# Optimization experiments

Hardware: AMD Instinct MI355X
Metric: run time of the kernel (lower is better)

Reference implementation:

```python
import jax, jax.numpy as jnp
import numpy as np

T_FRAMES = 8          # hardcoded in forward: T = int(8)
MAX_DISP = 3          # Correlation(kernel_size=1, max_displacement=3)
NUM_HEADS = 8
EPS = 1e-12           # F.normalize default eps


def setup_inputs() -> dict:
    key = jax.random.key(0)
    k1, k2, k3 = jax.random.split(key, 3)
    B, N, C = 2, 8192, 512  # N = T*H*W = 8*32*32
    x = jax.random.normal(k1, (B, N, C), jnp.float32)
    w_qkv = jax.random.normal(k2, (3 * C, C), jnp.float32) * (C ** -0.5)
    w_proj = jax.random.normal(k3, (C, C), jnp.float32) * (C ** -0.5)
    b_proj = jnp.zeros((C,), jnp.float32)
    return {"x": x, "w_qkv": w_qkv, "w_proj": w_proj, "b_proj": b_proj}


def _correlation(q, k, max_disp):
    # FlowNet-style cost volume, kernel_size=1: for each displacement (dy,dx)
    # in [-max_disp, max_disp]^2, mean over channels of q[.,h,w]*k[.,h+dy,w+dx],
    # out-of-bounds reads of k are zero. q,k: (b, d, H, W) -> (b, (2m+1)^2, H, W)
    b, d, H, W = q.shape
    kpad = jnp.pad(k, ((0, 0), (0, 0), (max_disp, max_disp), (max_disp, max_disp)))
    outs = []
    for dy in range(2 * max_disp + 1):
        for dx in range(2 * max_disp + 1):
            ks = kpad[:, :, dy:dy + H, dx:dx + W]
            outs.append(jnp.sum(q * ks, axis=1))
    return jnp.stack(outs, axis=1) / d


def _l2norm_ch(x):
    # normalize over channel axis 1 (F.normalize(dim=1))
    n = jnp.sqrt(jnp.sum(x * x, axis=1, keepdims=True))
    return x / jnp.maximum(n, EPS)


def reference(x, w_qkv, w_proj, b_proj):
    B, N, C = x.shape
    heads = NUM_HEADS
    hd = C // heads
    T = T_FRAMES
    H = int(round((N // T) ** 0.5)); W = H
    U = (2 * MAX_DISP + 1) ** 2  # 49

    qkv = (x @ w_qkv.T).reshape(B, N, 3, heads, hd).transpose(2, 0, 3, 1, 4)
    q, k, v = qkv[0], qkv[1], qkv[2]  # (B, heads, N, hd)

    # (b n) t d h w layout
    q = q.reshape(B * heads, T, H, W, hd).transpose(0, 1, 4, 2, 3)
    k = k.reshape(B * heads, T, H, W, hd).transpose(0, 1, 4, 2, 3)
    v = v.reshape(B * heads * T, H * W, hd)

    # k_postfix: shift k one frame earlier in time, repeat last frame
    k_post = jnp.concatenate([k[:, 1:], k[:, -1:]], axis=1)

    qf = _l2norm_ch(q.reshape(B * heads * T, hd, H, W))
    kf = _l2norm_ch(k_post.reshape(B * heads * T, hd, H, W))

    corr = _correlation(qf, kf, MAX_DISP).reshape(B * heads * T, U, H * W)
    # motion_attn = corr^T @ corr over the displacement axis, softmax over keys
    attn = jax.nn.softmax(jnp.einsum('bui,buj->bij', corr, corr), axis=-1)
    out = jnp.einsum('bij,bjd->bid', attn, v)  # (B*heads*T, H*W, hd)

    out = out.reshape(B, heads, T * H * W, hd).transpose(0, 2, 1, 3).reshape(B, N, C)
    return out @ w_proj.T + b_proj
```

## Files before the change

### kernel.cpp

```cpp
#include <hip/hip_runtime.h>
#include <hip/hip_bf16.h>
#include <stdint.h>


#define DEVFN __device__ __forceinline__

typedef __attribute__((ext_vector_type(8))) short bf16x8;
typedef __attribute__((ext_vector_type(4))) short s16x4;
typedef __attribute__((ext_vector_type(4))) float f32x4;

DEVFN float bf2f(short s) {
  union { unsigned int u; float f; } v;
  v.u = ((unsigned int)(unsigned short)s) << 16;
  return v.f;
}
DEVFN short f2bf(float f) {
  __hip_bfloat16 h = __float2bfloat16(f);
  return *reinterpret_cast<short*>(&h);
}

DEVFN void gl_lds16(const void* g, void* l) {
  __builtin_amdgcn_global_load_lds((const __attribute__((address_space(1))) void*)g,
                                   (__attribute__((address_space(3))) void*)l, 16, 0, 0);
}

#define MFMA(a, b, c) __builtin_amdgcn_mfma_f32_16x16x32_bf16((a), (b), (c), 0, 0, 0)

#define NTOK 8192
#define HW   1024

__global__ void k_cvt3(const float* __restrict__ x, const float* __restrict__ wq,
                       const float* __restrict__ wp, short* __restrict__ xb,
                       short* __restrict__ wqb, short* __restrict__ wpb) {
  int pid = blockIdx.x;
  const float* in; short* out; int i;
  if (pid < 4096)      { in = x;  out = xb;  i = pid * 256 + threadIdx.x; }
  else if (pid < 4480) { in = wq; out = wqb; i = (pid - 4096) * 256 + threadIdx.x; }
  else                 { in = wp; out = wpb; i = (pid - 4480) * 256 + threadIdx.x; }
  const float4* p = (const float4*)in + (size_t)i * 2;
  float4 a = p[0], b = p[1];
  bf16x8 r;
  r[0]=f2bf(a.x); r[1]=f2bf(a.y); r[2]=f2bf(a.z); r[3]=f2bf(a.w);
  r[4]=f2bf(b.x); r[5]=f2bf(b.y); r[6]=f2bf(b.z); r[7]=f2bf(b.w);
  *(bf16x8*)(out + (size_t)i * 8) = r;
}

template<int F32OUT>
__global__ __launch_bounds__(256, 2) void k_gemm_bt(
    const short* __restrict__ A, const short* __restrict__ Bm,
    void* __restrict__ Cp, const float* __restrict__ bias, int M, int N, int K)
{
  __shared__ short lA[128 * 64];
  __shared__ short lB[128 * 64];
  const int tid = threadIdx.x;
  const int lane = tid & 63, w = tid >> 6;
  const int wm = w >> 1, wn = w & 1;
  const int r15 = lane & 15, hi = (lane >> 4) * 16, g4 = (lane >> 4) * 4;
  const int pid = blockIdx.x;
  const int m0 = ((pid & 7) * 16 + ((pid >> 3) & 15)) * 128;
  const int n0 = (pid >> 7) * 128;

  f32x4 acc[4][4];
#pragma unroll
  for (int i = 0; i < 4; i++)
#pragma unroll
    for (int j = 0; j < 4; j++) acc[i][j] = (f32x4)0.f;

  for (int k0 = 0; k0 < K; k0 += 64) {
#pragma unroll
    for (int it = 0; it < 4; it++) {
      int chunk = it * 256 + tid;
      int row = chunk >> 3;
      int sb = ((chunk & 7) * 16) ^ ((row & 7) << 4);
      const char* srcA = (const char*)(A + (size_t)(m0 + row) * K + k0) + sb;
      const char* srcB = (const char*)(Bm + (size_t)(n0 + row) * K + k0) + sb;
      gl_lds16(srcA, lA + (it * 256 + w * 64) * 8);
      gl_lds16(srcB, lB + (it * 256 + w * 64) * 8);
    }
    asm volatile("s_waitcnt vmcnt(0)" ::: "memory");
    __syncthreads();

    bf16x8 af[4][2], bfr[4][2];
#pragma unroll
    for (int mt = 0; mt < 4; mt++) {
      int row = wm * 64 + mt * 16 + r15;
#pragma unroll
      for (int kh = 0; kh < 2; kh++) {
        int off = row * 128 + ((kh * 64 + hi) ^ ((row & 7) << 4));
        af[mt][kh] = *(const bf16x8*)((const char*)lA + off);
      }
    }
#pragma unroll
    for (int nt = 0; nt < 4; nt++) {
      int row = wn * 64 + nt * 16 + r15;
#pragma unroll
      for (int kh = 0; kh < 2; kh++) {
        int off = row * 128 + ((kh * 64 + hi) ^ ((row & 7) << 4));
        bfr[nt][kh] = *(const bf16x8*)((const char*)lB + off);
      }
    }
#pragma unroll
    for (int mt = 0; mt < 4; mt++)
#pragma unroll
      for (int nt = 0; nt < 4; nt++) {
        acc[mt][nt] = MFMA(af[mt][0], bfr[nt][0], acc[mt][nt]);
        acc[mt][nt] = MFMA(af[mt][1], bfr[nt][1], acc[mt][nt]);
      }
    __syncthreads();
  }

#pragma unroll
  for (int mt = 0; mt < 4; mt++)
#pragma unroll
    for (int j = 0; j < 4; j++) {
      int row = m0 + wm * 64 + mt * 16 + g4 + j;
#pragma unroll
      for (int nt = 0; nt < 4; nt++) {
        int col = n0 + wn * 64 + nt * 16 + r15;
        float v = acc[mt][nt][j];
        if (F32OUT) ((float*)Cp)[(size_t)row * N + col] = v + bias[col];
        else        ((short*)Cp)[(size_t)row * N + col] = f2bf(v);
      }
    }
}

__global__ __launch_bounds__(256, 4) void k_norm(short* __restrict__ qkvb) {
  const int tid = threadIdx.x;
  const int pid = blockIdx.x;
  const int xcd = pid & 7, idx = pid >> 3;
  const int g = 2 * xcd + (idx & 1);
  const int slice = (idx >> 1) & 1;
  const int iblk = idx >> 2;
#pragma unroll 1
  for (int pass = 0; pass < 8; ++pass) {
    int unit = pass * 32 + (tid >> 3);
    int i = iblk * 32 + (unit >> 3);
    int h = unit & 7;
    size_t addr = ((size_t)(g * HW + i)) * 1536 + slice * 512 + h * 64 + (tid & 7) * 8;
    bf16x8 d = *(const bf16x8*)(qkvb + addr);
    float ss = 0.f;
#pragma unroll
    for (int e = 0; e < 8; e++) { float f = bf2f(d[e]); ss += f * f; }
    ss += __shfl_xor(ss, 1); ss += __shfl_xor(ss, 2); ss += __shfl_xor(ss, 4);
    float sc = 1.f / (8.f * fmaxf(sqrtf(ss), 1e-12f));
    bf16x8 o;
#pragma unroll
    for (int e = 0; e < 8; e++) o[e] = f2bf(bf2f(d[e]) * sc);
    *(bf16x8*)(qkvb + addr) = o;
  }
}

__global__ __launch_bounds__(512, 4) void k_corr(
    const short* __restrict__ qkvb, short* __restrict__ corrI, short* __restrict__ corrU)
{
  __shared__ short stg[2560 * 8];
  __shared__ short scr[28 * 256];

  const int tid = threadIdx.x;
  const int lane = tid & 63, w = tid >> 6;
  const int r15 = lane & 15, hi = (lane >> 4) * 16, g4 = (lane >> 4) * 4;
  const int pid = blockIdx.x;
  const int xcd = pid & 7, idx = pid >> 3;
  const int g = 2 * xcd + (idx & 1);
  const int head = (idx >> 1) & 7;
  const int y0 = (idx >> 4) * 2;
  const int b = g >> 3, tf = g & 7;
  const int bht = b * 64 + head * 8 + tf;
  const int tk = (tf < 7) ? tf + 1 : 7;
  const size_t qbase = ((size_t)(g * HW)) * 1536 + head * 64;
  const size_t kbase = ((size_t)((b * 8 + tk) * HW)) * 1536 + 512 + head * 64;

#pragma unroll
  for (int i = 0; i < 5; i++) {
    int c = i * 512 + tid;
    int row = c >> 3;
    int sb = ((c & 7) * 16) ^ ((row & 7) << 4);
    short* dst = stg + (i * 512 + w * 64) * 8;
    if (i == 0) {
      int j = c >> 8, px = (c >> 3) & 31;
      gl_lds16((const char*)(qkvb + qbase + (size_t)((y0 + j) * 32 + px) * 1536) + sb, dst);
    } else {
      int c2 = c - 512;
      int slot = c2 >> 8, px = (c2 >> 3) & 31;
      int r = y0 - 3 + slot;
      if (r >= 0 && r < 32)
        gl_lds16((const char*)(qkvb + kbase + (size_t)(r * 32 + px) * 1536) + sb, dst);
      else
        *(bf16x8*)(stg + (size_t)c * 8) = (bf16x8)(short)0;
    }
  }
  asm volatile("s_waitcnt vmcnt(0)" ::: "memory");
  __syncthreads();

#pragma unroll 1
  for (int j = 0; j < 2; j++) {
    const int y = y0 + j;
    if (w < 7) {
      bf16x8 aq[2][2];
#pragma unroll
      for (int mt = 0; mt < 2; mt++) {
        int row = j * 32 + mt * 16 + r15;
#pragma unroll
        for (int kh = 0; kh < 2; kh++) {
          int off = row * 128 + ((kh * 64 + hi) ^ ((row & 7) << 4));
          aq[mt][kh] = *(const bf16x8*)((const char*)stg + off);
        }
      }
#pragma unroll
      for (int c = 0; c < 4; c++) {
        int t = w * 4 + c, nt = t >> 1, mt = t & 1;
        int dy = nt >> 1, xh = nt & 1;
        int slot = dy + j;
        int xx = xh * 16 + r15;
        int rowB = 64 + slot * 32 + xx;
        f32x4 a = (f32x4)0.f;
#pragma unroll
        for (int kh = 0; kh < 2; kh++) {
          int off = rowB * 128 + ((kh * 64 + hi) ^ ((rowB & 7) << 4));
          bf16x8 bb = *(const bf16x8*)((const char*)stg + off);
          a = MFMA(aq[mt][kh], bb, a);
        }
        s16x4 pk;
        pk[0] = f2bf(a[0]); pk[1] = f2bf(a[1]); pk[2] = f2bf(a[2]); pk[3] = f2bf(a[3]);
        *(s16x4*)(scr + t * 256 + r15 * 16 + g4) = pk;
      }
    }
    __syncthreads();

    if (tid < 256) {
      int x = tid >> 3, u0 = (tid & 7) * 8;
      bf16x8 o;
#pragma unroll
      for (int e = 0; e < 8; e++) {
        int u = u0 + e;
        int dy = u >> 3, dx = u & 7;
        int xx = x + dx - 3;
        int dyc = (dy > 6) ? 6 : dy;
        int t2 = (dyc * 2 + ((xx & 31) >> 4)) * 2 + (x >> 4);
        short vv = scr[t2 * 256 + (xx & 15) * 16 + (x & 15)];
        bool ok = (dx < 7) && (dy < 7) && (xx >= 0) && (xx < 32);
        short res = ok ? vv : (short)0;
        o[e] = (u == 63) ? (short)0x3F80 : res;
      }
      *(bf16x8*)(corrI + ((size_t)bht * HW + y * 32 + x) * 64 + u0) = o;
    } else {
      int tt = tid - 256;
      int u = tt >> 2, x0 = (tt & 3) * 8;
      int dy = u >> 3, dx = u & 7;
      int dyc = (dy > 6) ? 6 : dy;
      bf16x8 o;
#pragma unroll
      for (int e = 0; e < 8; e++) {
        int x = x0 + e;
        int xx = x + dx - 3;
        int t2 = (dyc * 2 + ((xx & 31) >> 4)) * 2 + (x >> 4);
        short vv = scr[t2 * 256 + (xx & 15) * 16 + (x & 15)];
        bool ok = (dx < 7) && (dy < 7) && (xx >= 0) && (xx < 32);
        short res = ok ? vv : (short)0;
        o[e] = (u == 63) ? (short)0x3F80 : res;
      }
      *(bf16x8*)(corrU + (size_t)bht * 65536 + u * HW + y * 32 + x0) = o;
    }
    __syncthreads();
  }
}

__global__ __launch_bounds__(256, 2) void k_vT(const short* __restrict__ qkvb, short* __restrict__ vT)
{
  __shared__ short lt[128 * 72];
  const int tid = threadIdx.x;
  const int pid = blockIdx.x;
  const int xcd = pid & 7, idx = pid >> 3;
  const int g = 2 * xcd + (idx & 1);
  const int head = (idx >> 1) & 7;
  const int cbase = (idx >> 4) * 256;
  const int b = g >> 3, tf = g & 7;
  const int bht = b * 64 + head * 8 + tf;
  const size_t rowbase = ((size_t)(g * HW)) * 1536 + 1024 + head * 64;
  for (int c0 = cbase; c0 < cbase + 256; c0 += 128) {
    __syncthreads();
#pragma unroll
    for (int it = 0; it < 4; it++) {
      int idx2 = it * 256 + tid;
      int row = idx2 >> 3, part = idx2 & 7;
      bf16x8 v = *(const bf16x8*)(qkvb + rowbase + (size_t)(c0 + row) * 1536 + part * 8);
      *(bf16x8*)(lt + row * 72 + part * 8) = v;
    }
    __syncthreads();
    int d = tid & 63, blk = tid >> 6;
#pragma unroll
    for (int qq = 0; qq < 4; qq++) {
      bf16x8 o;
#pragma unroll
      for (int e = 0; e < 8; e++) o[e] = lt[(blk * 32 + qq * 8 + e) * 72 + d];
      *(bf16x8*)(vT + ((size_t)bht * 64 + d) * HW + c0 + blk * 32 + qq * 8) = o;
    }
  }
}

__global__ __launch_bounds__(256, 2) void k_attn(
    const short* __restrict__ corrU, const short* __restrict__ corrI,
    const short* __restrict__ vT, short* __restrict__ out_attn)
{
  __shared__ short lV[32 * 64];
  __shared__ short lU[64 * 64];
  __shared__ short GTl[32 * 72];
  __shared__ float cl[64];
  __shared__ float cpart[256];
  const int tid = threadIdx.x, lane = tid & 63, w = tid >> 6;
  const int r15 = lane & 15, hi = (lane >> 4) * 16, g4 = (lane >> 4) * 4, g8 = (lane >> 4) * 8;
  const int pid = blockIdx.x;
  const int xcd = pid & 7, idx = pid >> 3;
  const int g = 2 * xcd + (idx & 1);
  const int head = (idx >> 1) & 7;
  const int dh = (idx >> 4) & 1;
  const int b = g >> 3, tf = g & 7;
  const int bht = b * 64 + head * 8 + tf;
  const int wm = w & 1, wn2 = (w >> 1) * 2;

  f32x4 accP[2];
  accP[0] = (f32x4)0.f; accP[1] = (f32x4)0.f;
  float c1p = 0.f;
  const short* vbase = vT + ((size_t)bht * 64 + dh * 32) * HW;
  const short* ubase = corrU + (size_t)bht * 65536;

  for (int i0 = 0; i0 < 1024; i0 += 64) {
    { int row = tid >> 3;
      int sb = ((tid & 7) * 16) ^ ((row & 7) << 4);
      gl_lds16((const char*)(vbase + (size_t)row * HW + i0) + sb, lV + (w * 64) * 8);
    }
#pragma unroll
    for (int it = 0; it < 2; it++) {
      int chunk = it * 256 + tid;
      int row = chunk >> 3;
      int sb = ((chunk & 7) * 16) ^ ((row & 7) << 4);
      gl_lds16((const char*)(ubase + (size_t)row * HW + i0) + sb, lU + (it * 256 + w * 64) * 8);
    }
    asm volatile("s_waitcnt vmcnt(0)" ::: "memory");
    __syncthreads();
    bf16x8 av[2];
    int rowA = wm * 16 + r15;
#pragma unroll
    for (int kh = 0; kh < 2; kh++) {
      int off = rowA * 128 + ((kh * 64 + hi) ^ ((rowA & 7) << 4));
      av[kh] = *(const bf16x8*)((const char*)lV + off);
    }
#pragma unroll
    for (int c = 0; c < 2; c++) {
      int rowB = (wn2 + c) * 16 + r15;
#pragma unroll
      for (int kh = 0; kh < 2; kh++) {
        int off = rowB * 128 + ((kh * 64 + hi) ^ ((rowB & 7) << 4));
        bf16x8 bu = *(const bf16x8*)((const char*)lU + off);
        accP[c] = MFMA(av[kh], bu, accP[c]);
      }
    }
    { int u = tid >> 2, partc = tid & 3;
#pragma unroll
      for (int h = 0; h < 2; h++) {
        int off = u * 128 + ((partc * 32 + h * 16) ^ ((u & 7) << 4));
        bf16x8 vv = *(const bf16x8*)((const char*)lU + off);
#pragma unroll
        for (int e = 0; e < 8; e++) c1p += bf2f(vv[e]);
      }
    }
    __syncthreads();
  }
  cpart[tid] = c1p;
#pragma unroll
  for (int c = 0; c < 2; c++)
#pragma unroll
    for (int j = 0; j < 4; j++) {
      int d = wm * 16 + g4 + j, u = (wn2 + c) * 16 + r15;
      GTl[d * 72 + u] = f2bf(accP[c][j]);
    }
  __syncthreads();
  if (tid < 64) cl[tid] = cpart[4 * tid] + cpart[4 * tid + 1] + cpart[4 * tid + 2] + cpart[4 * tid + 3];
  __syncthreads();

  bf16x8 gtb[2][2];
#pragma unroll
  for (int nt = 0; nt < 2; nt++)
#pragma unroll
    for (int kh = 0; kh < 2; kh++)
      gtb[nt][kh] = *(const bf16x8*)((const char*)GTl + (nt * 16 + r15) * 144 + kh * 64 + hi);

  float c1r[2][8];
#pragma unroll
  for (int kh = 0; kh < 2; kh++)
#pragma unroll
    for (int e = 0; e < 8; e++) c1r[kh][e] = cl[kh * 32 + g8 + e];

  const short* ibase = corrI + (size_t)bht * HW * 64;
  for (int s = 0; s < 16; s++) {
    int i0 = w * 256 + s * 16;
    bf16x8 af[2];
#pragma unroll
    for (int kh = 0; kh < 2; kh++)
      af[kh] = *(const bf16x8*)(ibase + (size_t)(i0 + r15) * 64 + kh * 32 + g8);
    f32x4 a2[2];
    a2[0] = (f32x4)0.f; a2[1] = (f32x4)0.f;
#pragma unroll
    for (int nt = 0; nt < 2; nt++)
#pragma unroll
      for (int kh = 0; kh < 2; kh++) a2[nt] = MFMA(af[kh], gtb[nt][kh], a2[nt]);

    float dp = 0.f;
#pragma unroll
    for (int kh = 0; kh < 2; kh++)
#pragma unroll
      for (int e = 0; e < 8; e++) dp += bf2f(af[kh][e]) * c1r[kh][e];
    dp += __shfl_xor(dp, 16);
    dp += __shfl_xor(dp, 32);

#pragma unroll
    for (int j = 0; j < 4; j++) {
      float dj = __shfl(dp, g4 + j);
      float inv = 1.f / dj;
      int i = i0 + g4 + j;
      size_t outrow = ((size_t)(g * HW + i)) * 512 + head * 64 + dh * 32;
#pragma unroll
      for (int nt = 0; nt < 2; nt++)
        out_attn[outrow + nt * 16 + r15] = f2bf(a2[nt][j] * inv);
    }
  }
}

extern "C" void kernel_launch(void* const* d_in, const int* in_sizes, int n_in,
                              void* d_out, int out_size, void* d_ws, size_t ws_size,
                              hipStream_t stream) {
  (void)in_sizes; (void)n_in; (void)out_size; (void)ws_size;
  const float* x      = (const float*)d_in[0];
  const float* w_qkv  = (const float*)d_in[1];
  const float* w_proj = (const float*)d_in[2];
  const float* b_proj = (const float*)d_in[3];

  char* ws = (char*)d_ws;
  short* qkvb   = (short*)(ws);
  short* xb     = (short*)(ws + 50331648);
  short* corrU  = (short*)(ws + 67108864);
  short* vT     = (short*)(ws + 83886080);
  short* wqkvb  = (short*)(ws + 100663296);
  short* wprojb = (short*)(ws + 102236160);
  short* corrI    = xb;
  short* out_attn = qkvb;

  k_cvt3<<<dim3(4608), 256, 0, stream>>>(x, w_qkv, w_proj, xb, wqkvb, wprojb);

  k_gemm_bt<0><<<dim3(1536), 256, 0, stream>>>(xb, wqkvb, qkvb, nullptr, 16384, 1536, 512);

  k_norm<<<dim3(1024), 256, 0, stream>>>(qkvb);

  k_corr<<<dim3(2048), 512, 0, stream>>>(qkvb, corrI, corrU);
  k_vT<<<dim3(512), 256, 0, stream>>>(qkvb, vT);

  k_attn<<<dim3(256), 256, 0, stream>>>(corrU, corrI, vT, out_attn);

  k_gemm_bt<1><<<dim3(512), 256, 0, stream>>>(out_attn, wprojb, d_out, b_proj, 16384, 512, 512);
}
```

Measured before the change: 121.5 us.

## Fuse L2 norm into QKV GEMM epilogue and V transpose into corr kernel

The per-head L2 normalization of q and k moves into the QKV GEMM epilogue, where the accumulators are reduced across lanes with shuffles before conversion to bf16. The V transpose moves into the tail of the correlation kernel, which stages V rows into LDS with a direct global-to-LDS load and writes them out transposed. This removes two kernel launches and one full read/write pass over the qkv buffer. In exchange, normalization now runs on fp32 accumulators rather than rounded bf16 values, and the correlation kernel does extra work at its end.

```diff
diff --git a/kernel.cpp b/kernel.cpp
--- a/kernel.cpp
+++ b/kernel.cpp
@@ -109,6 +109,22 @@
     __syncthreads();
   }
 
+  if (F32OUT == 0 && n0 < 1024) {
+#pragma unroll
+    for (int mt = 0; mt < 4; mt++)
+#pragma unroll
+      for (int j = 0; j < 4; j++) {
+        float ss = 0.f;
+#pragma unroll
+        for (int nt = 0; nt < 4; nt++) ss += acc[mt][nt][j] * acc[mt][nt][j];
+        ss += __shfl_xor(ss, 1); ss += __shfl_xor(ss, 2);
+        ss += __shfl_xor(ss, 4); ss += __shfl_xor(ss, 8);
+        float sc = 1.f / (8.f * fmaxf(sqrtf(ss), 1e-12f));
+#pragma unroll
+        for (int nt = 0; nt < 4; nt++) acc[mt][nt][j] *= sc;
+      }
+  }
+
 #pragma unroll
   for (int mt = 0; mt < 4; mt++)
 #pragma unroll
@@ -124,34 +140,9 @@
     }
 }
 
-__global__ __launch_bounds__(256, 4) void k_norm(short* __restrict__ qkvb) {
-  const int tid = threadIdx.x;
-  const int pid = blockIdx.x;
-  const int xcd = pid & 7, idx = pid >> 3;
-  const int g = 2 * xcd + (idx & 1);
-  const int slice = (idx >> 1) & 1;
-  const int iblk = idx >> 2;
-#pragma unroll 1
-  for (int pass = 0; pass < 8; ++pass) {
-    int unit = pass * 32 + (tid >> 3);
-    int i = iblk * 32 + (unit >> 3);
-    int h = unit & 7;
-    size_t addr = ((size_t)(g * HW + i)) * 1536 + slice * 512 + h * 64 + (tid & 7) * 8;
-    bf16x8 d = *(const bf16x8*)(qkvb + addr);
-    float ss = 0.f;
-#pragma unroll
-    for (int e = 0; e < 8; e++) { float f = bf2f(d[e]); ss += f * f; }
-    ss += __shfl_xor(ss, 1); ss += __shfl_xor(ss, 2); ss += __shfl_xor(ss, 4);
-    float sc = 1.f / (8.f * fmaxf(sqrtf(ss), 1e-12f));
-    bf16x8 o;
-#pragma unroll
-    for (int e = 0; e < 8; e++) o[e] = f2bf(bf2f(d[e]) * sc);
-    *(bf16x8*)(qkvb + addr) = o;
-  }
-}
-
 __global__ __launch_bounds__(512, 4) void k_corr(
-    const short* __restrict__ qkvb, short* __restrict__ corrI, short* __restrict__ corrU)
+    const short* __restrict__ qkvb, short* __restrict__ corrI,
+    short* __restrict__ corrU, short* __restrict__ vT)
 {
   __shared__ short stg[2560 * 8];
   __shared__ short scr[28 * 256];
@@ -263,38 +254,22 @@
     }
     __syncthreads();
   }
-}
-
-__global__ __launch_bounds__(256, 2) void k_vT(const short* __restrict__ qkvb, short* __restrict__ vT)
-{
-  __shared__ short lt[128 * 72];
-  const int tid = threadIdx.x;
-  const int pid = blockIdx.x;
-  const int xcd = pid & 7, idx = pid >> 3;
-  const int g = 2 * xcd + (idx & 1);
-  const int head = (idx >> 1) & 7;
-  const int cbase = (idx >> 4) * 256;
-  const int b = g >> 3, tf = g & 7;
-  const int bht = b * 64 + head * 8 + tf;
-  const size_t rowbase = ((size_t)(g * HW)) * 1536 + 1024 + head * 64;
-  for (int c0 = cbase; c0 < cbase + 256; c0 += 128) {
-    __syncthreads();
-#pragma unroll
-    for (int it = 0; it < 4; it++) {
-      int idx2 = it * 256 + tid;
-      int row = idx2 >> 3, part = idx2 & 7;
-      bf16x8 v = *(const bf16x8*)(qkvb + rowbase + (size_t)(c0 + row) * 1536 + part * 8);
-      *(bf16x8*)(lt + row * 72 + part * 8) = v;
-    }
-    __syncthreads();
-    int d = tid & 63, blk = tid >> 6;
-#pragma unroll
-    for (int qq = 0; qq < 4; qq++) {
-      bf16x8 o;
-#pragma unroll
-      for (int e = 0; e < 8; e++) o[e] = lt[(blk * 32 + qq * 8 + e) * 72 + d];
-      *(bf16x8*)(vT + ((size_t)bht * 64 + d) * HW + c0 + blk * 32 + qq * 8) = o;
-    }
+
+  {
+    int c = tid;
+    int i = c >> 3;
+    gl_lds16((const char*)(qkvb + ((size_t)(g * HW + y0 * 32 + i)) * 1536 + 1024 + head * 64)
+                 + (c & 7) * 16,
+             scr + (w * 64) * 8);
+  }
+  asm volatile("s_waitcnt vmcnt(0)" ::: "memory");
+  __syncthreads();
+  {
+    int d = tid >> 3, i0w = (tid & 7) * 8;
+    bf16x8 o;
+#pragma unroll
+    for (int e = 0; e < 8; e++) o[e] = scr[(i0w + e) * 64 + d];
+    *(bf16x8*)(vT + ((size_t)bht * 64 + d) * HW + y0 * 32 + i0w) = o;
   }
 }
 
@@ -449,10 +424,7 @@
 
   k_gemm_bt<0><<<dim3(1536), 256, 0, stream>>>(xb, wqkvb, qkvb, nullptr, 16384, 1536, 512);
 
-  k_norm<<<dim3(1024), 256, 0, stream>>>(qkvb);
-
-  k_corr<<<dim3(2048), 512, 0, stream>>>(qkvb, corrI, corrU);
-  k_vT<<<dim3(512), 256, 0, stream>>>(qkvb, vT);
+  k_corr<<<dim3(2048), 512, 0, stream>>>(qkvb, corrI, corrU, vT);
 
   k_attn<<<dim3(256), 256, 0, stream>>>(corrU, corrI, vT, out_attn);
 
```

Result: faster. 111.7 us, median of 2 (-8.1%).
